# Kernel optimization log

Measured on AMD Instinct MI355X. Metric: run time of the kernel, lower is better.

## Reference

```python
import jax
import jax.numpy as jnp
from jax import lax
import numpy as np

NUM_LABELS = 128
PAD, BOS, EOS = 0, 1, 2
B, T = 512, 512
NEG = -10000.0


def setup_inputs() -> dict:
    key = jax.random.key(0)
    k1, k2, k3, k4 = jax.random.split(key, 4)
    features = jax.random.normal(k1, (B, T, NUM_LABELS), dtype=jnp.float32)
    tag_seqs = jax.random.randint(k2, (B, T), 0, NUM_LABELS, dtype=jnp.int32)
    # prefix-valid mask with variable lengths in [T//2, T]
    lengths = jax.random.randint(k3, (B,), T // 2, T + 1, dtype=jnp.int32)
    mask = jnp.arange(T, dtype=jnp.int32)[None, :] < lengths[:, None]
    # transitions: randn then the constrained rows/cols from CRF.__init__
    tr = jax.random.normal(k4, (NUM_LABELS, NUM_LABELS), dtype=jnp.float32)
    tr = tr.at[:, BOS].set(NEG)
    tr = tr.at[EOS, :].set(NEG)
    tr = tr.at[PAD, :].set(NEG)
    tr = tr.at[:, PAD].set(NEG)
    tr = tr.at[PAD, PAD].set(0.0)
    tr = tr.at[PAD, EOS].set(0.0)
    return {"features": features, "tag_seqs": tag_seqs, "mask": mask, "transitions": tr}


def _crf_nll(features, transitions, tag_seqs, mask):
    maskf = mask.astype(features.dtype)  # [B,T]
    # ---- gold path score (score_sentences), fully vectorized over time ----
    emis = jnp.take_along_axis(features, tag_seqs[..., None], axis=-1)[..., 0]  # [B,T]
    trans_steps = transitions[tag_seqs[:, :-1], tag_seqs[:, 1:]]               # [B,T-1]
    gold = emis[:, 0] + transitions[BOS, tag_seqs[:, 0]]
    gold = gold + jnp.sum(maskf[:, 1:] * (emis[:, 1:] + trans_steps), axis=1)
    vlen = jnp.sum(mask.astype(jnp.int32), axis=1) - 1                          # [B]
    last_lab = jnp.take_along_axis(tag_seqs, vlen[:, None], axis=1)[:, 0]
    gold = gold + transitions[last_lab, EOS]
    # ---- log-partition (forward_alg): sequential scan over time ----
    init = transitions[BOS, :][None, :] + features[:, 0]  # [B,L]

    def step(fv, xs):
        feat_t, m_t = xs  # [B,L], [B] bool
        # scores[b, prev, cur] = fv[b,prev] + trans[prev,cur] + emit[b,cur]
        scores = fv[:, :, None] + transitions[None, :, :] + feat_t[:, None, :]
        new_fv = jax.nn.logsumexp(scores, axis=1)  # [B,L]
        fv = jnp.where(m_t[:, None], new_fv, fv)
        return fv, None

    xs = (jnp.swapaxes(features[:, 1:], 0, 1), jnp.swapaxes(mask[:, 1:], 0, 1))
    fv, _ = lax.scan(step, init, xs)
    logZ = jax.nn.logsumexp(fv + transitions[:, EOS][None, :], axis=-1)  # [B]
    return -jnp.mean(gold - logZ)


def reference(features, tag_seqs, mask, transitions):
    return _crf_nll(features, transitions, tag_seqs, mask)
```

## Files before the change

kernel.cpp:

```cpp
#include <hip/hip_runtime.h>
#include <cstdint>
#include <cstddef>

#define NLAB 128
#define TT   512
#define BB   512
#define MB   16
#define PAD_ 0
#define BOS_ 1
#define EOS_ 2
#define LN2F  0.6931471805599453f
#define LOG2E 1.4426950408889634f

typedef float f32x4 __attribute__((ext_vector_type(4)));
typedef short s16x8 __attribute__((ext_vector_type(8)));

#if __has_builtin(__builtin_amdgcn_exp2f)
#define EXP2F(x) __builtin_amdgcn_exp2f(x)
#else
#define EXP2F(x) exp2f(x)
#endif

#if __has_builtin(__builtin_amdgcn_sched_barrier)
#define SCHED_FENCE() __builtin_amdgcn_sched_barrier(0)
#else
#define SCHED_FENCE() asm volatile("" ::: "memory")
#endif

#define WAVE_BARRIER() do {                                                   \
    asm volatile("s_waitcnt lgkmcnt(0)" ::: "memory");                        \
    SCHED_FENCE();                                                            \
    __builtin_amdgcn_s_barrier();                                             \
    SCHED_FENCE();                                                            \
} while (0)

#define MFMA_(A,B,CV) __builtin_amdgcn_mfma_f32_16x16x32_bf16((A),(B),(CV),0,0,0)

__device__ __forceinline__ bool mask_is_i32(const unsigned char* m8) {
    return m8[1] == 0;
}
__device__ __forceinline__ bool mask_at(const unsigned char* m8, int idx, bool isi) {
    if (isi) return ((const int*)m8)[idx] != 0;
    return m8[idx] != 0;
}

__device__ __forceinline__ unsigned f2bf(float f) {
    union { float f; unsigned u; } v; v.f = f;
    return (v.u + 0x7FFFu + ((v.u >> 16) & 1u)) >> 16;
}
__device__ __forceinline__ unsigned cvtpk(float lo, float hi) {
    unsigned r;
    asm("v_cvt_pk_bf16_f32 %0, %1, %2" : "=v"(r) : "v"(lo), "v"(hi));
    return r;
}

__global__ __launch_bounds__(256, 1) void crf_fused(
        const float* __restrict__ feats,
        const int*   __restrict__ tags,
        const unsigned char* __restrict__ m8,
        const float* __restrict__ tr,
        float* __restrict__ gold_out,
        float* __restrict__ logZ_out) {
    const int bx  = blockIdx.x;
    const int tid = threadIdx.x;
    const bool isi = mask_is_i32(m8);

    if (bx >= BB / MB) {
        const int b    = (bx - BB / MB) * 4 + (tid >> 6);
        const int lane = tid & 63;
        const size_t fb = (size_t)b * TT * NLAB;
        float gp = 0.f; int cnt = 0;
        for (int tt = lane; tt < TT; tt += 64) {
            const int idx = b * TT + tt;
            const bool mm = mask_at(m8, idx, isi);
            cnt += mm ? 1 : 0;
            const int tg = tags[idx];
            if (tt == 0) gp += feats[fb + tg] + tr[BOS_ * NLAB + tg];
            else if (mm) gp += feats[fb + (size_t)tt * NLAB + tg]
                             + tr[tags[idx - 1] * NLAB + tg];
        }
        #pragma unroll
        for (int off = 32; off > 0; off >>= 1) {
            gp  += __shfl_xor(gp,  off, 64);
            cnt += __shfl_xor(cnt, off, 64);
        }
        if (lane == 0)
            gold_out[b] = gp + tr[tags[b * TT + cnt - 1] * NLAB + EOS_];
        return;
    }

    const int w = tid >> 6;
    const int l = tid & 63;
    const int a = l >> 4;
    const int c = l & 15;
    const int G = bx * MB + c;
    const size_t fbase = (size_t)G * TT * NLAB;

    __shared__ __align__(16) unsigned short P16[2][2048];
    __shared__ float red_s[4][MB];

    const int s0 = 4 * w + a, s1 = 4 * w + 16 + a;

    f32x4 F0a, F0b, F1a, F1b, F2a, F2b, F3a, F3b,
          F4a, F4b, F5a, F5b, F6a, F6b, F7a, F7b;
    {
        const f32x4* fp = (const f32x4*)(feats + fbase);
        F0a = fp[1 * 32 + s0]; F0b = fp[1 * 32 + s1];
        F1a = fp[2 * 32 + s0]; F1b = fp[2 * 32 + s1];
        F2a = fp[3 * 32 + s0]; F2b = fp[3 * 32 + s1];
        F3a = fp[4 * 32 + s0]; F3b = fp[4 * 32 + s1];
        F4a = fp[5 * 32 + s0]; F4b = fp[5 * 32 + s1];
        F5a = fp[6 * 32 + s0]; F5b = fp[6 * 32 + s1];
        F6a = fp[7 * 32 + s0]; F6b = fp[7 * 32 + s1];
        F7a = fp[8 * 32 + s0]; F7b = fp[8 * 32 + s1];
    }

    int cnt = 0;
    if (isi) {
        const uint4* mp = (const uint4*)((const int*)m8 + (size_t)G * TT + a * 128);
        #pragma unroll 8
        for (int i = 0; i < 32; ++i) {
            uint4 v = mp[i];
            cnt += (v.x != 0) + (v.y != 0) + (v.z != 0) + (v.w != 0);
        }
    } else {
        const uint4* mp = (const uint4*)(m8 + (size_t)G * TT + a * 128);
        #pragma unroll
        for (int i = 0; i < 8; ++i) {
            uint4 v = mp[i];
            cnt += (int)((((v.x & 0x01010101u) * 0x01010101u) >> 24)
                       + (((v.y & 0x01010101u) * 0x01010101u) >> 24)
                       + (((v.z & 0x01010101u) * 0x01010101u) >> 24)
                       + (((v.w & 0x01010101u) * 0x01010101u) >> 24));
        }
    }
    cnt += __shfl_xor(cnt, 16, 64);
    cnt += __shfl_xor(cnt, 32, 64);
    const int mylen = cnt;
    int maxlen = mylen;
    maxlen = max(maxlen, __shfl_xor(maxlen, 1, 64));
    maxlen = max(maxlen, __shfl_xor(maxlen, 2, 64));
    maxlen = max(maxlen, __shfl_xor(maxlen, 4, 64));
    maxlen = max(maxlen, __shfl_xor(maxlen, 8, 64));
    const int mx = maxlen - 1;

    s16x8 Af00, Af01, Af02, Af03, Af10, Af11, Af12, Af13;
    {
        s16x8* A0[4] = {&Af00, &Af01, &Af02, &Af03};
        s16x8* A1[4] = {&Af10, &Af11, &Af12, &Af13};
        #pragma unroll
        for (int kt = 0; kt < 4; ++kt)
            #pragma unroll
            for (int jj = 0; jj < 8; ++jj) {
                const float* tp = tr + (kt * 32 + a * 8 + jj) * NLAB + c;
                (*A0[kt])[jj] = (short)f2bf(__expf(tp[w * 16]));
                (*A1[kt])[jj] = (short)f2bf(__expf(tp[(w + 4) * 16]));
            }
    }

    f32x4 pf0, pf1;
    float C;
    {
        const float n0 = tr[BOS_ * NLAB + 3] + feats[fbase + 3];
        C = n0;
        const f32x4 tb0 = *(const f32x4*)(tr + BOS_ * NLAB + w * 16 + a * 4);
        const f32x4 ff0 = *(const f32x4*)(feats + fbase + w * 16 + a * 4);
        const f32x4 tb1 = *(const f32x4*)(tr + BOS_ * NLAB + (w + 4) * 16 + a * 4);
        const f32x4 ff1 = *(const f32x4*)(feats + fbase + (w + 4) * 16 + a * 4);
        #pragma unroll
        for (int r = 0; r < 4; ++r) {
            pf0[r] = __expf(tb0[r] + ff0[r] - n0);
            pf1[r] = __expf(tb1[r] + ff1[r] - n0);
        }
    }

    const int wb0 = ((2 * w       + (a >> 1)) * 16 + c) * 8 + (a & 1) * 4;
    const int wb1 = ((2 * (w + 4) + (a >> 1)) * 16 + c) * 8 + (a & 1) * 4;
    *(uint2*)&P16[0][wb0] = make_uint2(cvtpk(pf0[0], pf0[1]), cvtpk(pf0[2], pf0[3]));
    *(uint2*)&P16[0][wb1] = make_uint2(cvtpk(pf1[0], pf1[1]), cvtpk(pf1[2], pf1[3]));
    __syncthreads();

    const int rab = a * 16 + c;
    const f32x4 zac = {0.f, 0.f, 0.f, 0.f};

#define STEP(T_, Fa, Fb) {                                                    \
    const int PB = (T_) & 1;                                                  \
    const s16x8* PR = (const s16x8*)P16[1 - PB];                              \
    const s16x8 b0 = PR[rab],       b1 = PR[64 + rab],                        \
                b2 = PR[128 + rab], b3 = PR[192 + rab];                       \
    const int p3 = (int)P16[1 - PB][c * 8 + 3];                               \
    const int e = ((p3 >> 7) & 255) - 126;                                    \
    f32x4 x0 = MFMA_(Af00, b0, zac); x0 = MFMA_(Af01, b1, x0);                \
    f32x4 y0 = MFMA_(Af02, b2, zac); y0 = MFMA_(Af03, b3, y0);                \
    f32x4 x1 = MFMA_(Af10, b0, zac); x1 = MFMA_(Af11, b1, x1);                \
    f32x4 y1 = MFMA_(Af12, b2, zac); y1 = MFMA_(Af13, b3, y1);                \
    const float sc = __uint_as_float((unsigned)(127 - e) << 23);    \
    const f32x4 acc0 = x0 + y0, acc1 = x1 + y1;                               \
    const bool live = (T_) < mylen;                                           \
    _Pragma("unroll")                                                         \
    for (int r = 0; r < 4; ++r) {                                             \
        const float q0 = acc0[r] * (EXP2F(Fa[r] * LOG2E) * sc);               \
        const float q1 = acc1[r] * (EXP2F(Fb[r] * LOG2E) * sc);               \
        if (live) { pf0[r] = q0; pf1[r] = q1; }                               \
    }                                                                         \
    if (live) C += (float)e * LN2F;                                           \
    *(uint2*)&P16[PB][wb0] = make_uint2(cvtpk(pf0[0], pf0[1]),                \
                                        cvtpk(pf0[2], pf0[3]));               \
    *(uint2*)&P16[PB][wb1] = make_uint2(cvtpk(pf1[0], pf1[1]),                \
                                        cvtpk(pf1[2], pf1[3]));               \
    WAVE_BARRIER();                                                           \
}

    #pragma unroll 1
    for (int t0 = 1; t0 < maxlen; t0 += 8) {
        const int nstep = maxlen - t0;
        STEP(t0, F0a, F0b)
        if (nstep > 1) STEP(t0 + 1, F1a, F1b)
        if (nstep > 2) STEP(t0 + 2, F2a, F2b)
        if (nstep > 3) STEP(t0 + 3, F3a, F3b)
        if (nstep > 4) STEP(t0 + 4, F4a, F4b)
        if (nstep > 5) STEP(t0 + 5, F5a, F5b)
        if (nstep > 6) STEP(t0 + 6, F6a, F6b)
        if (nstep > 7) STEP(t0 + 7, F7a, F7b)
        if (t0 + 8 < maxlen) {
            const f32x4* fp;
#define RF(i, Xa, Xb)                                                         \
            fp = (const f32x4*)(feats + fbase                                 \
                     + (size_t)min(t0 + 8 + (i), mx) * NLAB);                 \
            Xa = fp[s0]; Xb = fp[s1];
            RF(0, F0a, F0b) RF(1, F1a, F1b) RF(2, F2a, F2b) RF(3, F3a, F3b)
            RF(4, F4a, F4b) RF(5, F5a, F5b) RF(6, F6a, F6b) RF(7, F7a, F7b)
#undef RF
        }
    }
#undef STEP

    float s = 0.f;
    #pragma unroll
    for (int r = 0; r < 4; ++r) {
        s += pf0[r] * __expf(tr[(w * 16 + 4 * a + r) * NLAB + EOS_]);
        s += pf1[r] * __expf(tr[((w + 4) * 16 + 4 * a + r) * NLAB + EOS_]);
    }
    s += __shfl_xor(s, 16, 64);
    s += __shfl_xor(s, 32, 64);
    if (l < 16) red_s[w][c] = s;
    __syncthreads();
    if (tid < 16) {
        float S = red_s[0][tid] + red_s[1][tid] + red_s[2][tid] + red_s[3][tid];
        logZ_out[bx * MB + tid] = C + __logf(S);
    }
}

__global__ void crf_finalize(const float* __restrict__ gold,
                             const float* __restrict__ logZ,
                             float* __restrict__ out) {
    __shared__ float sh[4];
    const int i = threadIdx.x;
    float v = (logZ[i] - gold[i]) + (logZ[i + 256] - gold[i + 256]);
    #pragma unroll
    for (int off = 32; off > 0; off >>= 1)
        v += __shfl_xor(v, off, 64);
    if ((i & 63) == 0) sh[i >> 6] = v;
    __syncthreads();
    if (i == 0) out[0] = (sh[0] + sh[1] + sh[2] + sh[3]) * (1.0f / (float)BB);
}

extern "C" void kernel_launch(void* const* d_in, const int* in_sizes, int n_in,
                              void* d_out, int out_size, void* d_ws, size_t ws_size,
                              hipStream_t stream) {
    const float*         feats = (const float*)d_in[0];
    const int*           tags  = (const int*)d_in[1];
    const unsigned char* m8    = (const unsigned char*)d_in[2];
    const float*         tr    = (const float*)d_in[3];

    float* gold = (float*)d_ws;
    float* logZ = gold + BB;
    float* out  = (float*)d_out;

    hipLaunchKernelGGL(crf_fused, dim3(BB / MB + BB / 4), dim3(256), 0, stream,
                       feats, tags, m8, tr, gold, logZ);
    hipLaunchKernelGGL(crf_finalize, dim3(1), dim3(256), 0, stream,
                       gold, logZ, out);
}
```

Before: 424.3 us.

## Precompute bf16 exp(emissions) in separate pass and run scan on one wave

Adds a preprocessing kernel that converts all emissions to exp() in bf16, written in an MFMA-friendly layout in workspace. The scan kernel then runs a single 64-lane wave per group of 16 sequences and keeps the whole state in registers, passing it between MFMA steps without LDS round-trips or block barriers. Each step only multiplies by the precomputed emission exponentials. This trades an extra full pass over the features (64MB read, 32MB write) and bf16 rounding of the emissions for a shorter serial critical path per timestep. The original kernel is kept as a fallback when the workspace is too small.

```diff
diff --git a/kernel.cpp b/kernel.cpp
--- a/kernel.cpp
+++ b/kernel.cpp
@@ -12,6 +12,9 @@
 #define LN2F  0.6931471805599453f
 #define LOG2E 1.4426950408889634f
 
+#define EF_OFF   4096
+#define EF_BYTES ((size_t)BB * TT * NLAB * 2)
+
 typedef float f32x4 __attribute__((ext_vector_type(4)));
 typedef short s16x8 __attribute__((ext_vector_type(8)));
 
@@ -43,7 +46,6 @@
     if (isi) return ((const int*)m8)[idx] != 0;
     return m8[idx] != 0;
 }
-
 __device__ __forceinline__ unsigned f2bf(float f) {
     union { float f; unsigned u; } v; v.f = f;
     return (v.u + 0x7FFFu + ((v.u >> 16) & 1u)) >> 16;
@@ -54,7 +56,207 @@
     return r;
 }
 
-__global__ __launch_bounds__(256, 1) void crf_fused(
+
+__global__ __launch_bounds__(256) void crf_ef(const float* __restrict__ feats,
+                                              unsigned short* __restrict__ ef) {
+    const size_t gid = (size_t)blockIdx.x * 256 + threadIdx.x;
+    const int    k8  = (int)(gid & 15);
+    const size_t bt  = gid >> 4;
+    const int L0 = k8 * 8;
+    const float4 f0 = *(const float4*)(feats + bt * NLAB + L0);
+    const float4 f1 = *(const float4*)(feats + bt * NLAB + L0 + 4);
+    const int mt = L0 >> 4, q0 = (L0 >> 2) & 3;
+    const int b  = (int)(bt >> 9);
+    const int bx = b >> 4, cc = b & 15;
+    const int t  = (int)(bt & 511);
+    const size_t base = (size_t)((size_t)(bx * TT + t) * 4) << 9;
+    const unsigned a0 = cvtpk(__expf(f0.x), __expf(f0.y));
+    const unsigned a1 = cvtpk(__expf(f0.z), __expf(f0.w));
+    const unsigned b0 = cvtpk(__expf(f1.x), __expf(f1.y));
+    const unsigned b1 = cvtpk(__expf(f1.z), __expf(f1.w));
+    *(uint2*)(ef + base + ((size_t)q0       << 9) + (cc << 5) + (mt << 2)) = make_uint2(a0, a1);
+    *(uint2*)(ef + base + ((size_t)(q0 + 1) << 9) + (cc << 5) + (mt << 2)) = make_uint2(b0, b1);
+}
+
+__global__ __launch_bounds__(64, 1) void crf_scan(
+        const float* __restrict__ feats,
+        const int*   __restrict__ tags,
+        const unsigned char* __restrict__ m8,
+        const float* __restrict__ tr,
+        const unsigned short* __restrict__ ef,
+        float* __restrict__ gold_out,
+        float* __restrict__ logZ_out) {
+    const int bx  = blockIdx.x;
+    const int tid = threadIdx.x;
+    const bool isi = mask_is_i32(m8);
+
+    if (bx >= BB / MB) {
+        const int b    = bx - BB / MB;
+        const int lane = tid;
+        const size_t fb = (size_t)b * TT * NLAB;
+        float gp = 0.f; int cnt = 0;
+        for (int tt = lane; tt < TT; tt += 64) {
+            const int idx = b * TT + tt;
+            const bool mm = mask_at(m8, idx, isi);
+            cnt += mm ? 1 : 0;
+            const int tg = tags[idx];
+            if (tt == 0) gp += feats[fb + tg] + tr[BOS_ * NLAB + tg];
+            else if (mm) gp += feats[fb + (size_t)tt * NLAB + tg]
+                             + tr[tags[idx - 1] * NLAB + tg];
+        }
+        #pragma unroll
+        for (int off = 32; off > 0; off >>= 1) {
+            gp  += __shfl_xor(gp,  off, 64);
+            cnt += __shfl_xor(cnt, off, 64);
+        }
+        if (lane == 0)
+            gold_out[b] = gp + tr[tags[b * TT + cnt - 1] * NLAB + EOS_];
+        return;
+    }
+
+    const int q  = tid >> 4;
+    const int cc = tid & 15;
+    const int G  = bx * MB + cc;
+    const size_t fbase = (size_t)G * TT * NLAB;
+
+    int cnt = 0;
+    if (isi) {
+        const uint4* mp = (const uint4*)((const int*)m8 + (size_t)G * TT + q * 128);
+        #pragma unroll 8
+        for (int i = 0; i < 32; ++i) {
+            uint4 v = mp[i];
+            cnt += (v.x != 0) + (v.y != 0) + (v.z != 0) + (v.w != 0);
+        }
+    } else {
+        const uint4* mp = (const uint4*)(m8 + (size_t)G * TT + q * 128);
+        #pragma unroll
+        for (int i = 0; i < 8; ++i) {
+            uint4 v = mp[i];
+            cnt += (int)((((v.x & 0x01010101u) * 0x01010101u) >> 24)
+                       + (((v.y & 0x01010101u) * 0x01010101u) >> 24)
+                       + (((v.z & 0x01010101u) * 0x01010101u) >> 24)
+                       + (((v.w & 0x01010101u) * 0x01010101u) >> 24));
+        }
+    }
+    cnt += __shfl_xor(cnt, 16, 64);
+    cnt += __shfl_xor(cnt, 32, 64);
+    const int mylen = cnt;
+    int maxlen = mylen;
+    maxlen = max(maxlen, __shfl_xor(maxlen, 1, 64));
+    maxlen = max(maxlen, __shfl_xor(maxlen, 2, 64));
+    maxlen = max(maxlen, __shfl_xor(maxlen, 4, 64));
+    maxlen = max(maxlen, __shfl_xor(maxlen, 8, 64));
+
+    s16x8 Af[8][4];
+    #pragma unroll
+    for (int kt = 0; kt < 4; ++kt)
+        #pragma unroll
+        for (int jj = 0; jj < 8; ++jj) {
+            const int mu = kt * 32 + (jj >> 2) * 16 + q * 4 + (jj & 3);
+            const float* tp = tr + mu * NLAB + cc;
+            #pragma unroll
+            for (int mt = 0; mt < 8; ++mt)
+                Af[mt][kt][jj] = (short)f2bf(__expf(tp[mt * 16]));
+        }
+
+    float pf[8][4];
+    float C;
+    {
+        const float n0 = tr[BOS_ * NLAB + 3] + feats[fbase + 3];
+        C = n0;
+        #pragma unroll
+        for (int mt = 0; mt < 8; ++mt) {
+            const float4 tb = *(const float4*)(tr + BOS_ * NLAB + mt * 16 + q * 4);
+            const float4 ff = *(const float4*)(feats + fbase + mt * 16 + q * 4);
+            pf[mt][0] = __expf(tb.x + ff.x - n0);
+            pf[mt][1] = __expf(tb.y + ff.y - n0);
+            pf[mt][2] = __expf(tb.z + ff.z - n0);
+            pf[mt][3] = __expf(tb.w + ff.w - n0);
+        }
+    }
+
+    union BF { uint4 u; s16x8 v; };
+    BF bf0, bf1, bf2, bf3;
+#define PACK_B() {                                                            \
+    bf0.u = make_uint4(cvtpk(pf[0][0], pf[0][1]), cvtpk(pf[0][2], pf[0][3]),  \
+                       cvtpk(pf[1][0], pf[1][1]), cvtpk(pf[1][2], pf[1][3])); \
+    bf1.u = make_uint4(cvtpk(pf[2][0], pf[2][1]), cvtpk(pf[2][2], pf[2][3]),  \
+                       cvtpk(pf[3][0], pf[3][1]), cvtpk(pf[3][2], pf[3][3])); \
+    bf2.u = make_uint4(cvtpk(pf[4][0], pf[4][1]), cvtpk(pf[4][2], pf[4][3]),  \
+                       cvtpk(pf[5][0], pf[5][1]), cvtpk(pf[5][2], pf[5][3])); \
+    bf3.u = make_uint4(cvtpk(pf[6][0], pf[6][1]), cvtpk(pf[6][2], pf[6][3]),  \
+                       cvtpk(pf[7][0], pf[7][1]), cvtpk(pf[7][2], pf[7][3])); \
+}
+    PACK_B();
+
+    const unsigned short* efp = ef + (((size_t)(bx * TT) * 4 + q) << 9) + (cc << 5);
+    uint4 S00, S01, S02, S03, S10, S11, S12, S13,
+          S20, S21, S22, S23, S30, S31, S32, S33;
+#define LDEF(T_, A0, A1, A2, A3) {                                            \
+    const uint4* p_ = (const uint4*)(efp + ((size_t)(T_) << 11));             \
+    A0 = p_[0]; A1 = p_[1]; A2 = p_[2]; A3 = p_[3]; }
+    LDEF(1, S00, S01, S02, S03)
+    LDEF(2, S10, S11, S12, S13)
+    LDEF(3, S20, S21, S22, S23)
+    LDEF(4, S30, S31, S32, S33)
+
+    int e_bc = 0;
+    const f32x4 zac = {0.f, 0.f, 0.f, 0.f};
+
+#define CMP_(V,J) ((J)==0?(V).x:(J)==1?(V).y:(J)==2?(V).z:(V).w)
+#define PKC(P, E0,E1,E2,E3) ((P)<4 ? CMP_(E0,(P)&3) : (P)<8 ? CMP_(E1,(P)&3) \
+                           : (P)<12 ? CMP_(E2,(P)&3) : CMP_(E3,(P)&3))
+
+#define STEP(T_, A0, A1, A2, A3) {                                            \
+    const uint4 e0_ = A0, e1_ = A1, e2_ = A2, e3_ = A3;                       \
+    LDEF(min((T_) + 4, TT - 1), A0, A1, A2, A3)                               \
+    SCHED_FENCE();                                                            \
+    const float sc = __uint_as_float((unsigned)(127 - e_bc) << 23); \
+    const bool live = (T_) < mylen;                                           \
+    _Pragma("unroll")                                                         \
+    for (int mt = 0; mt < 8; ++mt) {                                          \
+        f32x4 x = MFMA_(Af[mt][0], bf0.v, zac); x = MFMA_(Af[mt][1], bf1.v, x); \
+        f32x4 y = MFMA_(Af[mt][2], bf2.v, zac); y = MFMA_(Af[mt][3], bf3.v, y); \
+        const f32x4 acc = x + y;                                              \
+        _Pragma("unroll")                                                     \
+        for (int h = 0; h < 2; ++h) {                                         \
+            const unsigned pk = PKC(mt * 2 + h, e0_, e1_, e2_, e3_);          \
+            const float fe0 = __uint_as_float(pk << 16);                      \
+            const float fe1 = __uint_as_float(pk & 0xffff0000u);              \
+            const float q0 = acc[2 * h]     * fe0 * sc;                       \
+            const float q1 = acc[2 * h + 1] * fe1 * sc;                       \
+            if (live) { pf[mt][2 * h] = q0; pf[mt][2 * h + 1] = q1; }         \
+        }                                                                     \
+    }                                                                         \
+    if (live) C += (float)e_bc * LN2F;                                        \
+    PACK_B();                                                                 \
+    const int el = (int)((__float_as_uint(pf[0][3]) >> 23) & 255u) - 126;     \
+    e_bc = __shfl(el, cc, 64);       \
+}
+
+    #pragma unroll 1
+    for (int t0 = 1; t0 < maxlen; t0 += 4) {
+        const int nstep = maxlen - t0;
+        STEP(t0, S00, S01, S02, S03)
+        if (nstep > 1) STEP(t0 + 1, S10, S11, S12, S13)
+        if (nstep > 2) STEP(t0 + 2, S20, S21, S22, S23)
+        if (nstep > 3) STEP(t0 + 3, S30, S31, S32, S33)
+    }
+#undef STEP
+#undef LDEF
+
+    float s = 0.f;
+    #pragma unroll
+    for (int mt = 0; mt < 8; ++mt)
+        #pragma unroll
+        for (int r = 0; r < 4; ++r)
+            s += pf[mt][r] * __expf(tr[(mt * 16 + 4 * q + r) * NLAB + EOS_]);
+    s += __shfl_xor(s, 16, 64);
+    s += __shfl_xor(s, 32, 64);
+    if (tid < 16) logZ_out[bx * MB + tid] = C + __logf(s);
+}
+
+__global__ __launch_bounds__(256, 1) void crf_fused_fb(
         const float* __restrict__ feats,
         const int*   __restrict__ tags,
         const unsigned char* __restrict__ m8,
@@ -183,7 +385,7 @@
     const int rab = a * 16 + c;
     const f32x4 zac = {0.f, 0.f, 0.f, 0.f};
 
-#define STEP(T_, Fa, Fb) {                                                    \
+#define STEPF(T_, Fa, Fb) {                                                   \
     const int PB = (T_) & 1;                                                  \
     const s16x8* PR = (const s16x8*)P16[1 - PB];                              \
     const s16x8 b0 = PR[rab],       b1 = PR[64 + rab],                        \
@@ -194,7 +396,7 @@
     f32x4 y0 = MFMA_(Af02, b2, zac); y0 = MFMA_(Af03, b3, y0);                \
     f32x4 x1 = MFMA_(Af10, b0, zac); x1 = MFMA_(Af11, b1, x1);                \
     f32x4 y1 = MFMA_(Af12, b2, zac); y1 = MFMA_(Af13, b3, y1);                \
-    const float sc = __uint_as_float((unsigned)(127 - e) << 23);    \
+    const float sc = __uint_as_float((unsigned)(127 - e) << 23);              \
     const f32x4 acc0 = x0 + y0, acc1 = x1 + y1;                               \
     const bool live = (T_) < mylen;                                           \
     _Pragma("unroll")                                                         \
@@ -214,14 +416,14 @@
     #pragma unroll 1
     for (int t0 = 1; t0 < maxlen; t0 += 8) {
         const int nstep = maxlen - t0;
-        STEP(t0, F0a, F0b)
-        if (nstep > 1) STEP(t0 + 1, F1a, F1b)
-        if (nstep > 2) STEP(t0 + 2, F2a, F2b)
-        if (nstep > 3) STEP(t0 + 3, F3a, F3b)
-        if (nstep > 4) STEP(t0 + 4, F4a, F4b)
-        if (nstep > 5) STEP(t0 + 5, F5a, F5b)
-        if (nstep > 6) STEP(t0 + 6, F6a, F6b)
-        if (nstep > 7) STEP(t0 + 7, F7a, F7b)
+        STEPF(t0, F0a, F0b)
+        if (nstep > 1) STEPF(t0 + 1, F1a, F1b)
+        if (nstep > 2) STEPF(t0 + 2, F2a, F2b)
+        if (nstep > 3) STEPF(t0 + 3, F3a, F3b)
+        if (nstep > 4) STEPF(t0 + 4, F4a, F4b)
+        if (nstep > 5) STEPF(t0 + 5, F5a, F5b)
+        if (nstep > 6) STEPF(t0 + 6, F6a, F6b)
+        if (nstep > 7) STEPF(t0 + 7, F7a, F7b)
         if (t0 + 8 < maxlen) {
             const f32x4* fp;
 #define RF(i, Xa, Xb)                                                         \
@@ -233,7 +435,7 @@
 #undef RF
         }
     }
-#undef STEP
+#undef STEPF
 
     float s = 0.f;
     #pragma unroll
@@ -277,8 +479,16 @@
     float* logZ = gold + BB;
     float* out  = (float*)d_out;
 
-    hipLaunchKernelGGL(crf_fused, dim3(BB / MB + BB / 4), dim3(256), 0, stream,
-                       feats, tags, m8, tr, gold, logZ);
+    if (ws_size >= EF_OFF + EF_BYTES) {
+        unsigned short* ef = (unsigned short*)((char*)d_ws + EF_OFF);
+        hipLaunchKernelGGL(crf_ef, dim3((BB * TT * MB) / 256), dim3(256), 0,
+                           stream, feats, ef);
+        hipLaunchKernelGGL(crf_scan, dim3(BB / MB + BB), dim3(64), 0, stream,
+                           feats, tags, m8, tr, ef, gold, logZ);
+    } else {
+        hipLaunchKernelGGL(crf_fused_fb, dim3(BB / MB + BB / 4), dim3(256), 0,
+                           stream, feats, tags, m8, tr, gold, logZ);
+    }
     hipLaunchKernelGGL(crf_finalize, dim3(1), dim3(256), 0, stream,
                        gold, logZ, out);
 }
```

After: 598.7 us. 41.1% more time.
